# Optimization experiments

Measured on AMD Instinct MI355X. Metric: run time of the kernel, lower is better.

The kernel has to match this reference:

```python
import jax, jax.numpy as jnp
import numpy as np

IN_DIM = 1024
HEAD_DIM = 64
NUM_HEADS = 16
SEQ = 4096


def setup_inputs() -> dict:
    key = jax.random.key(0)
    ks = jax.random.split(key, 7)
    s = 1.0 / np.sqrt(IN_DIM)
    return {
        "h": jax.random.normal(ks[0], (SEQ, IN_DIM), dtype=jnp.float32),
        "Wq": jax.random.uniform(ks[1], (IN_DIM, NUM_HEADS * HEAD_DIM), jnp.float32, -s, s),
        "Wk": jax.random.uniform(ks[2], (IN_DIM, NUM_HEADS * HEAD_DIM), jnp.float32, -s, s),
        "Wv": jax.random.uniform(ks[3], (IN_DIM, NUM_HEADS * HEAD_DIM), jnp.float32, -s, s),
        "bq": jax.random.uniform(ks[4], (NUM_HEADS * HEAD_DIM,), jnp.float32, -s, s),
        "bk": jax.random.uniform(ks[5], (NUM_HEADS * HEAD_DIM,), jnp.float32, -s, s),
        "bv": jax.random.uniform(ks[6], (NUM_HEADS * HEAD_DIM,), jnp.float32, -s, s),
    }


def reference(h, Wq, Wk, Wv, bq, bk, bv):
    n = h.shape[0]
    # QKV projections -> [H, S, D]
    q = (h @ Wq + bq).reshape(n, NUM_HEADS, HEAD_DIM).transpose(1, 0, 2)
    k = (h @ Wk + bk).reshape(n, NUM_HEADS, HEAD_DIM).transpose(1, 0, 2)
    v = (h @ Wv + bv).reshape(n, NUM_HEADS, HEAD_DIM).transpose(1, 0, 2)
    scale = 1.0 / np.sqrt(HEAD_DIM).astype(np.float32)
    scores = jnp.einsum('hsd,htd->hst', q, k) * scale  # [H, S, S]
    probs = jax.nn.softmax(scores, axis=-1)
    out = jnp.einsum('hst,htd->hsd', probs, v)  # [H, S, D]
    return out.transpose(1, 0, 2).reshape(n, NUM_HEADS * HEAD_DIM)
```

## Files before the change

### kernel.cpp

```cpp
#include <hip/hip_runtime.h>
#include <hip/hip_bf16.h>

#define IN_DIM    1024
#define HEAD_DIM  64
#define NUM_HEADS 16
#define SEQ       4096

#define QSCALE 0.18033688011112042f

typedef __bf16 bf16;
typedef __attribute__((ext_vector_type(4))) __bf16 bf16x4;
typedef __attribute__((ext_vector_type(8))) __bf16 bf16x8;
typedef __attribute__((ext_vector_type(4))) float floatx4;

__device__ __forceinline__ void async16(bf16* lds, const bf16* g) {
    __builtin_amdgcn_global_load_lds(
        (const __attribute__((address_space(1))) unsigned int*)g,
        (__attribute__((address_space(3))) unsigned int*)lds, 16, 0, 0);
}


__global__ void mha_conv_h(const float* __restrict__ h, bf16* __restrict__ hb) {
    int i = blockIdx.x * blockDim.x + threadIdx.x;
    float4 v = ((const float4*)h)[i];
    bf16x4 r;
    r[0] = (bf16)v.x; r[1] = (bf16)v.y; r[2] = (bf16)v.z; r[3] = (bf16)v.w;
    ((bf16x4*)hb)[i] = r;
}

__global__ void mha_conv_wt(const float* __restrict__ Wq, const float* __restrict__ Wk,
                            const float* __restrict__ Wv, bf16* __restrict__ Wt) {
    __shared__ bf16 tile[64][65];
    const int mat = blockIdx.z;
    const float* W = (mat == 0) ? Wq : (mat == 1) ? Wk : Wv;
    const int k0 = blockIdx.y * 64, n0 = blockIdx.x * 64;
    const int tn = threadIdx.x & 63, tq = threadIdx.x >> 6;
#pragma unroll
    for (int i = 0; i < 16; ++i) {
        int kk = tq + i * 4;
        tile[kk][tn] = (bf16)W[(size_t)(k0 + kk) * 1024 + n0 + tn];
    }
    __syncthreads();
#pragma unroll
    for (int i = 0; i < 16; ++i) {
        int nn = tq + i * 4;
        Wt[((size_t)mat << 20) + (size_t)(n0 + nn) * 1024 + k0 + tn] = tile[tn][nn];
    }
}

__launch_bounds__(256)
__global__ void mha_qkv_gemm(const bf16* __restrict__ hb, const bf16* __restrict__ Wt,
                             const float* __restrict__ bq, const float* __restrict__ bk,
                             const float* __restrict__ bv,
                             bf16* __restrict__ Qb, bf16* __restrict__ Kb,
                             bf16* __restrict__ Vt) {
    __shared__ __align__(16) bf16 As[128 * 32];
    __shared__ __align__(16) bf16 Bs[128 * 32];

    const int lane = threadIdx.x & 63;
    const int wave = threadIdx.x >> 6;
    const int l16  = lane & 15;
    const int quad = lane >> 4;
    const int wm   = wave & 1;
    const int wn   = wave >> 1;

    const int m0  = blockIdx.x * 128;
    const int n0  = blockIdx.y * 128;
    const int mat = n0 >> 10;
    const int nc0 = n0 & 1023;

    const bf16* Wp = Wt + ((size_t)mat << 20);

    floatx4 acc[4][4] = {};
    const int swz = (l16 >> 1) & 3;

    for (int k0 = 0; k0 < IN_DIM; k0 += 32) {
#pragma unroll
        for (int r = 0; r < 2; ++r) {
            int g = wave * 128 + r * 64 + lane;
            int row = g >> 2, c = g & 3;
            int gc = c ^ ((row >> 1) & 3);
            bf16* ldsbase_a = As + (size_t)(wave * 128 + r * 64) * 8;
            bf16* ldsbase_b = Bs + (size_t)(wave * 128 + r * 64) * 8;
            async16(ldsbase_a, hb + (size_t)(m0 + row) * IN_DIM + k0 + gc * 8);
            async16(ldsbase_b, Wp + (size_t)(nc0 + row) * IN_DIM + k0 + gc * 8);
        }
        __syncthreads();

        bf16x8 af[4], bf[4];
#pragma unroll
        for (int mt = 0; mt < 4; ++mt)
            af[mt] = *(const bf16x8*)(As + (size_t)(wm * 64 + mt * 16 + l16) * 32
                                      + ((quad ^ swz) * 8));
#pragma unroll
        for (int nt = 0; nt < 4; ++nt)
            bf[nt] = *(const bf16x8*)(Bs + (size_t)(wn * 64 + nt * 16 + l16) * 32
                                      + ((quad ^ swz) * 8));
#pragma unroll
        for (int mt = 0; mt < 4; ++mt)
#pragma unroll
            for (int nt = 0; nt < 4; ++nt)
                acc[mt][nt] = __builtin_amdgcn_mfma_f32_16x16x32_bf16(af[mt], bf[nt],
                                                                      acc[mt][nt], 0, 0, 0);
        __syncthreads();
    }

    const float* bias = (mat == 0) ? bq : (mat == 1) ? bk : bv;
#pragma unroll
    for (int nt = 0; nt < 4; ++nt) {
        int nc = nc0 + wn * 64 + nt * 16 + l16;
        float bb = bias[nc];
        int head = nc >> 6, d = nc & 63;
#pragma unroll
        for (int mt = 0; mt < 4; ++mt)
#pragma unroll
            for (int r = 0; r < 4; ++r) {
                int srow = m0 + wm * 64 + mt * 16 + quad * 4 + r;
                float v = acc[mt][nt][r] + bb;
                if (mat == 0)
                    Qb[((size_t)head * SEQ + srow) * HEAD_DIM + d] = (bf16)(v * QSCALE);
                else if (mat == 1)
                    Kb[((size_t)head * SEQ + srow) * HEAD_DIM + d] = (bf16)v;
                else
                    Vt[((size_t)head * HEAD_DIM + d) * SEQ + srow] = (bf16)v;
            }
    }
}

__launch_bounds__(512)
__global__ void mha_attn(const bf16* __restrict__ Qb, const bf16* __restrict__ Kb,
                         const bf16* __restrict__ Vt, float* __restrict__ out) {
    __shared__ __align__(16) bf16 Ks[2][64 * 64];
    __shared__ __align__(16) bf16 Vs[2][64 * 64];
    __shared__ __align__(16) bf16 Ps[8][16 * 72];

    const int lane = threadIdx.x & 63;
    const int wave = threadIdx.x >> 6;
    const int l16  = lane & 15;
    const int quad = lane >> 4;

    const int hh    = blockIdx.y;
    const int qbase = blockIdx.x * 128 + wave * 16;

    const bf16* Qh = Qb + (size_t)hh * SEQ * HEAD_DIM;
    const bf16* Kh = Kb + (size_t)hh * SEQ * HEAD_DIM;
    const bf16* Vh = Vt + (size_t)hh * HEAD_DIM * SEQ;

    const int sg   = wave * 64 + lane;
    const int srow = sg >> 3;
    const int sgc  = (sg & 7) ^ (srow & 7);

    bf16x8 qf[2];
#pragma unroll
    for (int ks = 0; ks < 2; ++ks)
        qf[ks] = *(const bf16x8*)(Qh + (size_t)(qbase + l16) * HEAD_DIM + ks * 32 + quad * 8);

    bf16x8 vone;
#pragma unroll
    for (int i = 0; i < 8; ++i) vone[i] = (bf16)1.0f;

    floatx4 o[4] = {};
    floatx4 ol   = {};

    bf16* lp = &Ps[wave][0];
    const int swk = l16 & 7;

    async16(&Ks[0][wave * 512], Kh + (size_t)srow * HEAD_DIM + sgc * 8);
    async16(&Vs[0][wave * 512], Vh + (size_t)srow * SEQ + sgc * 8);
    __syncthreads();

    for (int t0 = 0; t0 < SEQ; t0 += 64) {
        const int cur = (t0 >> 6) & 1, nxt = cur ^ 1;
        if (t0 + 64 < SEQ) {
            async16(&Ks[nxt][wave * 512], Kh + (size_t)(t0 + 64 + srow) * HEAD_DIM + sgc * 8);
            async16(&Vs[nxt][wave * 512], Vh + (size_t)srow * SEQ + t0 + 64 + sgc * 8);
        }

        bf16x8 kf[4][2], vf[4][2];
#pragma unroll
        for (int tt = 0; tt < 4; ++tt)
#pragma unroll
            for (int ks = 0; ks < 2; ++ks)
                kf[tt][ks] = *(const bf16x8*)(&Ks[cur][(size_t)(tt * 16 + l16) * 64
                                              + (((ks * 4 + quad) ^ swk) * 8)]);
#pragma unroll
        for (int dt = 0; dt < 4; ++dt)
#pragma unroll
            for (int ks = 0; ks < 2; ++ks)
                vf[dt][ks] = *(const bf16x8*)(&Vs[cur][(size_t)(dt * 16 + l16) * 64
                                              + (((ks * 4 + quad) ^ swk) * 8)]);

#pragma unroll
        for (int tt = 0; tt < 4; ++tt) {
            floatx4 s = {};
            s = __builtin_amdgcn_mfma_f32_16x16x32_bf16(kf[tt][0], qf[0], s, 0, 0, 0);
            s = __builtin_amdgcn_mfma_f32_16x16x32_bf16(kf[tt][1], qf[1], s, 0, 0, 0);
            bf16x4 pk;
#pragma unroll
            for (int r = 0; r < 4; ++r) pk[r] = (bf16)__builtin_amdgcn_exp2f(s[r]);
            *(bf16x4*)(lp + l16 * 72 + tt * 16 + quad * 4) = pk;
        }

#pragma unroll
        for (int ks = 0; ks < 2; ++ks) {
            bf16x8 pf = *(const bf16x8*)(lp + l16 * 72 + ks * 32 + quad * 8);
#pragma unroll
            for (int dt = 0; dt < 4; ++dt)
                o[dt] = __builtin_amdgcn_mfma_f32_16x16x32_bf16(pf, vf[dt][ks], o[dt], 0, 0, 0);
            ol = __builtin_amdgcn_mfma_f32_16x16x32_bf16(pf, vone, ol, 0, 0, 0);
        }
        __syncthreads();
    }

#pragma unroll
    for (int r = 0; r < 4; ++r) {
        float inv = 1.0f / ol[r];
        int srow_o = qbase + quad * 4 + r;
#pragma unroll
        for (int dt = 0; dt < 4; ++dt)
            out[(size_t)srow_o * (NUM_HEADS * HEAD_DIM) + hh * 64 + dt * 16 + l16]
                = o[dt][r] * inv;
    }
}

extern "C" void kernel_launch(void* const* d_in, const int* in_sizes, int n_in,
                              void* d_out, int out_size, void* d_ws, size_t ws_size,
                              hipStream_t stream) {
    const float* h  = (const float*)d_in[0];
    const float* Wq = (const float*)d_in[1];
    const float* Wk = (const float*)d_in[2];
    const float* Wv = (const float*)d_in[3];
    const float* bq = (const float*)d_in[4];
    const float* bk = (const float*)d_in[5];
    const float* bv = (const float*)d_in[6];
    float* out = (float*)d_out;

    char* ws = (char*)d_ws;
    const size_t MB = 1024 * 1024;
    bf16* hb = (bf16*)(ws);
    bf16* Wt = (bf16*)(ws + 8 * MB);
    bf16* Qb = (bf16*)(ws + 14 * MB);
    bf16* Kb = (bf16*)(ws + 22 * MB);
    bf16* Vt = (bf16*)(ws + 30 * MB);

    mha_conv_h<<<(SEQ * IN_DIM / 4) / 256, 256, 0, stream>>>(h, hb);
    mha_conv_wt<<<dim3(16, 16, 3), 256, 0, stream>>>(Wq, Wk, Wv, Wt);
    mha_qkv_gemm<<<dim3(SEQ / 128, (3 * IN_DIM) / 128), 256, 0, stream>>>(
        hb, Wt, bq, bk, bv, Qb, Kb, Vt);
    mha_attn<<<dim3(SEQ / 128, NUM_HEADS), 512, 0, stream>>>(Qb, Kb, Vt, out);
}
```

Before: 204.2 us.

## Software-pipeline attention S and PV stages, transpose V projection stores

The attention loop is restructured so the QK^T/exp stage for tile t runs alongside the PV stage for tile t-1. P uses double-buffered LDS and V uses a triple buffer, and K/V fragments are loaded from LDS just before use rather than up front, which lowers register pressure. Launch bounds now request 4 blocks per SM. Separately, the V projection swaps the MFMA operands so that Vt stores are contiguous along the sequence dimension instead of strided. The cost is more LDS use and more complex buffer indexing.

```diff
diff --git a/kernel.cpp b/kernel.cpp
--- a/kernel.cpp
+++ b/kernel.cpp
@@ -73,6 +73,7 @@
 
     floatx4 acc[4][4] = {};
     const int swz = (l16 >> 1) & 3;
+    const bool swap = (mat == 2);
 
     for (int k0 = 0; k0 < IN_DIM; k0 += 32) {
 #pragma unroll
@@ -96,43 +97,66 @@
         for (int nt = 0; nt < 4; ++nt)
             bf[nt] = *(const bf16x8*)(Bs + (size_t)(wn * 64 + nt * 16 + l16) * 32
                                       + ((quad ^ swz) * 8));
-#pragma unroll
-        for (int mt = 0; mt < 4; ++mt)
-#pragma unroll
-            for (int nt = 0; nt < 4; ++nt)
-                acc[mt][nt] = __builtin_amdgcn_mfma_f32_16x16x32_bf16(af[mt], bf[nt],
-                                                                      acc[mt][nt], 0, 0, 0);
+        if (!swap) {
+#pragma unroll
+            for (int mt = 0; mt < 4; ++mt)
+#pragma unroll
+                for (int nt = 0; nt < 4; ++nt)
+                    acc[mt][nt] = __builtin_amdgcn_mfma_f32_16x16x32_bf16(af[mt], bf[nt],
+                                                                          acc[mt][nt], 0, 0, 0);
+        } else {
+#pragma unroll
+            for (int mt = 0; mt < 4; ++mt)
+#pragma unroll
+                for (int nt = 0; nt < 4; ++nt)
+                    acc[mt][nt] = __builtin_amdgcn_mfma_f32_16x16x32_bf16(bf[nt], af[mt],
+                                                                          acc[mt][nt], 0, 0, 0);
+        }
         __syncthreads();
     }
 
-    const float* bias = (mat == 0) ? bq : (mat == 1) ? bk : bv;
-#pragma unroll
-    for (int nt = 0; nt < 4; ++nt) {
-        int nc = nc0 + wn * 64 + nt * 16 + l16;
-        float bb = bias[nc];
-        int head = nc >> 6, d = nc & 63;
-#pragma unroll
-        for (int mt = 0; mt < 4; ++mt)
+    if (!swap) {
+        const float* bias = (mat == 0) ? bq : bk;
+#pragma unroll
+        for (int nt = 0; nt < 4; ++nt) {
+            int nc = nc0 + wn * 64 + nt * 16 + l16;
+            float bb = bias[nc];
+            int head = nc >> 6, d = nc & 63;
+#pragma unroll
+            for (int mt = 0; mt < 4; ++mt)
+#pragma unroll
+                for (int r = 0; r < 4; ++r) {
+                    int srow = m0 + wm * 64 + mt * 16 + quad * 4 + r;
+                    float v = acc[mt][nt][r] + bb;
+                    if (mat == 0)
+                        Qb[((size_t)head * SEQ + srow) * HEAD_DIM + d] = (bf16)(v * QSCALE);
+                    else
+                        Kb[((size_t)head * SEQ + srow) * HEAD_DIM + d] = (bf16)v;
+                }
+        }
+    } else {
+#pragma unroll
+        for (int nt = 0; nt < 4; ++nt)
 #pragma unroll
             for (int r = 0; r < 4; ++r) {
-                int srow = m0 + wm * 64 + mt * 16 + quad * 4 + r;
-                float v = acc[mt][nt][r] + bb;
-                if (mat == 0)
-                    Qb[((size_t)head * SEQ + srow) * HEAD_DIM + d] = (bf16)(v * QSCALE);
-                else if (mat == 1)
-                    Kb[((size_t)head * SEQ + srow) * HEAD_DIM + d] = (bf16)v;
-                else
-                    Vt[((size_t)head * HEAD_DIM + d) * SEQ + srow] = (bf16)v;
+                int n = nc0 + wn * 64 + nt * 16 + quad * 4 + r;
+                float bb = bv[n];
+                int head = n >> 6, d = n & 63;
+#pragma unroll
+                for (int mt = 0; mt < 4; ++mt) {
+                    int s = m0 + wm * 64 + mt * 16 + l16;
+                    Vt[((size_t)head * 64 + d) * SEQ + s] = (bf16)(acc[mt][nt][r] + bb);
+                }
             }
     }
 }
 
-__launch_bounds__(512)
+__launch_bounds__(512, 4)
 __global__ void mha_attn(const bf16* __restrict__ Qb, const bf16* __restrict__ Kb,
                          const bf16* __restrict__ Vt, float* __restrict__ out) {
     __shared__ __align__(16) bf16 Ks[2][64 * 64];
-    __shared__ __align__(16) bf16 Vs[2][64 * 64];
-    __shared__ __align__(16) bf16 Ps[8][16 * 72];
+    __shared__ __align__(16) bf16 Vs[3][64 * 64];
+    __shared__ __align__(16) bf16 Ps[2][8][16 * 72];
 
     const int lane = threadIdx.x & 63;
     const int wave = threadIdx.x >> 6;
@@ -162,55 +186,65 @@
     floatx4 o[4] = {};
     floatx4 ol   = {};
 
-    bf16* lp = &Ps[wave][0];
     const int swk = l16 & 7;
 
-    async16(&Ks[0][wave * 512], Kh + (size_t)srow * HEAD_DIM + sgc * 8);
-    async16(&Vs[0][wave * 512], Vh + (size_t)srow * SEQ + sgc * 8);
-    __syncthreads();
-
-    for (int t0 = 0; t0 < SEQ; t0 += 64) {
-        const int cur = (t0 >> 6) & 1, nxt = cur ^ 1;
-        if (t0 + 64 < SEQ) {
-            async16(&Ks[nxt][wave * 512], Kh + (size_t)(t0 + 64 + srow) * HEAD_DIM + sgc * 8);
-            async16(&Vs[nxt][wave * 512], Vh + (size_t)srow * SEQ + t0 + 64 + sgc * 8);
-        }
-
-        bf16x8 kf[4][2], vf[4][2];
-#pragma unroll
-        for (int tt = 0; tt < 4; ++tt)
-#pragma unroll
-            for (int ks = 0; ks < 2; ++ks)
-                kf[tt][ks] = *(const bf16x8*)(&Ks[cur][(size_t)(tt * 16 + l16) * 64
-                                              + (((ks * 4 + quad) ^ swk) * 8)]);
-#pragma unroll
-        for (int dt = 0; dt < 4; ++dt)
-#pragma unroll
-            for (int ks = 0; ks < 2; ++ks)
-                vf[dt][ks] = *(const bf16x8*)(&Vs[cur][(size_t)(dt * 16 + l16) * 64
-                                              + (((ks * 4 + quad) ^ swk) * 8)]);
-
+    auto stageK = [&](int slot, int t) {
+        async16(&Ks[slot][wave * 512], Kh + (size_t)(t * 64 + srow) * HEAD_DIM + sgc * 8);
+    };
+    auto stageV = [&](int slot, int t) {
+        async16(&Vs[slot][wave * 512], Vh + (size_t)srow * SEQ + t * 64 + sgc * 8);
+    };
+    auto doS = [&](int kslot, int pslot) {
+        bf16* lp = &Ps[pslot][wave][0];
 #pragma unroll
         for (int tt = 0; tt < 4; ++tt) {
+            bf16x8 k0 = *(const bf16x8*)(&Ks[kslot][(size_t)(tt * 16 + l16) * 64
+                                         + ((quad ^ swk) * 8)]);
+            bf16x8 k1 = *(const bf16x8*)(&Ks[kslot][(size_t)(tt * 16 + l16) * 64
+                                         + (((4 + quad) ^ swk) * 8)]);
             floatx4 s = {};
-            s = __builtin_amdgcn_mfma_f32_16x16x32_bf16(kf[tt][0], qf[0], s, 0, 0, 0);
-            s = __builtin_amdgcn_mfma_f32_16x16x32_bf16(kf[tt][1], qf[1], s, 0, 0, 0);
+            s = __builtin_amdgcn_mfma_f32_16x16x32_bf16(k0, qf[0], s, 0, 0, 0);
+            s = __builtin_amdgcn_mfma_f32_16x16x32_bf16(k1, qf[1], s, 0, 0, 0);
             bf16x4 pk;
 #pragma unroll
             for (int r = 0; r < 4; ++r) pk[r] = (bf16)__builtin_amdgcn_exp2f(s[r]);
             *(bf16x4*)(lp + l16 * 72 + tt * 16 + quad * 4) = pk;
         }
-
+    };
+    auto doPV = [&](int vslot, int pslot) {
+        bf16* lp = &Ps[pslot][wave][0];
 #pragma unroll
         for (int ks = 0; ks < 2; ++ks) {
             bf16x8 pf = *(const bf16x8*)(lp + l16 * 72 + ks * 32 + quad * 8);
 #pragma unroll
-            for (int dt = 0; dt < 4; ++dt)
-                o[dt] = __builtin_amdgcn_mfma_f32_16x16x32_bf16(pf, vf[dt][ks], o[dt], 0, 0, 0);
+            for (int dt = 0; dt < 4; ++dt) {
+                bf16x8 vf = *(const bf16x8*)(&Vs[vslot][(size_t)(dt * 16 + l16) * 64
+                                             + (((ks * 4 + quad) ^ swk) * 8)]);
+                o[dt] = __builtin_amdgcn_mfma_f32_16x16x32_bf16(pf, vf, o[dt], 0, 0, 0);
+            }
             ol = __builtin_amdgcn_mfma_f32_16x16x32_bf16(pf, vone, ol, 0, 0, 0);
         }
+    };
+
+    stageK(0, 0); stageV(0, 0);
+    __syncthreads();
+
+    stageK(1, 1); stageV(1, 1);
+    doS(0, 0);
+    __syncthreads();
+
+    int ivw = 2;
+    int ivr = 0;
+    for (int t = 1; t < 64; ++t) {
+        const int par = t & 1;
+        if (t < 63) { stageK(par ^ 1, t + 1); stageV(ivw, t + 1); }
+        doS(par, par);
+        doPV(ivr, par ^ 1);
         __syncthreads();
-    }
+        ivw = (ivw == 2) ? 0 : ivw + 1;
+        ivr = (ivr == 2) ? 0 : ivr + 1;
+    }
+    doPV(0, 1);
 
 #pragma unroll
     for (int r = 0; r < 4; ++r) {
```

After: 220.1 us. 1.08x slower.

## Give each attention wave four query tiles and coalesce the V-transpose store

Applied to the files above, without the earlier changes.

The attention kernel now runs 256-thread blocks that each cover 256 queries, so every wave owns 64 query rows (four 16-row tiles). Each K/V fragment read from LDS is then reused across four tiles, which cuts LDS traffic and K/V staging per query. In the QKV GEMM, the V path swaps the MFMA operands so the accumulator comes out transposed, turning the strided Vt stores into contiguous writes along the sequence. The trade-off is more accumulator registers per wave and fewer blocks in the grid (256 instead of 512), which can reduce occupancy.

```diff
diff --git a/kernel.cpp b/kernel.cpp
--- a/kernel.cpp
+++ b/kernel.cpp
@@ -74,65 +74,102 @@
     floatx4 acc[4][4] = {};
     const int swz = (l16 >> 1) & 3;
 
-    for (int k0 = 0; k0 < IN_DIM; k0 += 32) {
-#pragma unroll
-        for (int r = 0; r < 2; ++r) {
-            int g = wave * 128 + r * 64 + lane;
-            int row = g >> 2, c = g & 3;
-            int gc = c ^ ((row >> 1) & 3);
-            bf16* ldsbase_a = As + (size_t)(wave * 128 + r * 64) * 8;
-            bf16* ldsbase_b = Bs + (size_t)(wave * 128 + r * 64) * 8;
-            async16(ldsbase_a, hb + (size_t)(m0 + row) * IN_DIM + k0 + gc * 8);
-            async16(ldsbase_b, Wp + (size_t)(nc0 + row) * IN_DIM + k0 + gc * 8);
-        }
-        __syncthreads();
-
-        bf16x8 af[4], bf[4];
-#pragma unroll
-        for (int mt = 0; mt < 4; ++mt)
-            af[mt] = *(const bf16x8*)(As + (size_t)(wm * 64 + mt * 16 + l16) * 32
-                                      + ((quad ^ swz) * 8));
+    int g0 = wave * 128 + lane, g1 = g0 + 64;
+    int row0 = g0 >> 2, gc0 = (g0 & 3) ^ ((row0 >> 1) & 3);
+    int row1 = g1 >> 2, gc1 = (g1 & 3) ^ ((row1 >> 1) & 3);
+    bf16* la0 = As + (size_t)(wave * 128) * 8;
+    bf16* la1 = As + (size_t)(wave * 128 + 64) * 8;
+    bf16* lb0 = Bs + (size_t)(wave * 128) * 8;
+    bf16* lb1 = Bs + (size_t)(wave * 128 + 64) * 8;
+
+    if (mat != 2) {
+        for (int k0 = 0; k0 < IN_DIM; k0 += 32) {
+            async16(la0, hb + (size_t)(m0 + row0) * IN_DIM + k0 + gc0 * 8);
+            async16(la1, hb + (size_t)(m0 + row1) * IN_DIM + k0 + gc1 * 8);
+            async16(lb0, Wp + (size_t)(nc0 + row0) * IN_DIM + k0 + gc0 * 8);
+            async16(lb1, Wp + (size_t)(nc0 + row1) * IN_DIM + k0 + gc1 * 8);
+            __syncthreads();
+            bf16x8 af[4], bf[4];
+#pragma unroll
+            for (int mt = 0; mt < 4; ++mt)
+                af[mt] = *(const bf16x8*)(As + (size_t)(wm * 64 + mt * 16 + l16) * 32
+                                          + ((quad ^ swz) * 8));
+#pragma unroll
+            for (int nt = 0; nt < 4; ++nt)
+                bf[nt] = *(const bf16x8*)(Bs + (size_t)(wn * 64 + nt * 16 + l16) * 32
+                                          + ((quad ^ swz) * 8));
+#pragma unroll
+            for (int mt = 0; mt < 4; ++mt)
+#pragma unroll
+                for (int nt = 0; nt < 4; ++nt)
+                    acc[mt][nt] = __builtin_amdgcn_mfma_f32_16x16x32_bf16(af[mt], bf[nt],
+                                                                          acc[mt][nt], 0, 0, 0);
+            __syncthreads();
+        }
+        const float* bias = (mat == 0) ? bq : bk;
+#pragma unroll
+        for (int nt = 0; nt < 4; ++nt) {
+            int nc = nc0 + wn * 64 + nt * 16 + l16;
+            float bb = bias[nc];
+            int head = nc >> 6, d = nc & 63;
+#pragma unroll
+            for (int mt = 0; mt < 4; ++mt)
+#pragma unroll
+                for (int r = 0; r < 4; ++r) {
+                    int srow = m0 + wm * 64 + mt * 16 + quad * 4 + r;
+                    float v = acc[mt][nt][r] + bb;
+                    if (mat == 0)
+                        Qb[((size_t)head * SEQ + srow) * HEAD_DIM + d] = (bf16)(v * QSCALE);
+                    else
+                        Kb[((size_t)head * SEQ + srow) * HEAD_DIM + d] = (bf16)v;
+                }
+        }
+    } else {
+        for (int k0 = 0; k0 < IN_DIM; k0 += 32) {
+            async16(la0, hb + (size_t)(m0 + row0) * IN_DIM + k0 + gc0 * 8);
+            async16(la1, hb + (size_t)(m0 + row1) * IN_DIM + k0 + gc1 * 8);
+            async16(lb0, Wp + (size_t)(nc0 + row0) * IN_DIM + k0 + gc0 * 8);
+            async16(lb1, Wp + (size_t)(nc0 + row1) * IN_DIM + k0 + gc1 * 8);
+            __syncthreads();
+            bf16x8 af[4], bf[4];
+#pragma unroll
+            for (int mt = 0; mt < 4; ++mt)
+                af[mt] = *(const bf16x8*)(As + (size_t)(wm * 64 + mt * 16 + l16) * 32
+                                          + ((quad ^ swz) * 8));
+#pragma unroll
+            for (int nt = 0; nt < 4; ++nt)
+                bf[nt] = *(const bf16x8*)(Bs + (size_t)(wn * 64 + nt * 16 + l16) * 32
+                                          + ((quad ^ swz) * 8));
+#pragma unroll
+            for (int mt = 0; mt < 4; ++mt)
+#pragma unroll
+                for (int nt = 0; nt < 4; ++nt)
+                    acc[mt][nt] = __builtin_amdgcn_mfma_f32_16x16x32_bf16(bf[nt], af[mt],
+                                                                          acc[mt][nt], 0, 0, 0);
+            __syncthreads();
+        }
 #pragma unroll
         for (int nt = 0; nt < 4; ++nt)
-            bf[nt] = *(const bf16x8*)(Bs + (size_t)(wn * 64 + nt * 16 + l16) * 32
-                                      + ((quad ^ swz) * 8));
-#pragma unroll
-        for (int mt = 0; mt < 4; ++mt)
-#pragma unroll
-            for (int nt = 0; nt < 4; ++nt)
-                acc[mt][nt] = __builtin_amdgcn_mfma_f32_16x16x32_bf16(af[mt], bf[nt],
-                                                                      acc[mt][nt], 0, 0, 0);
-        __syncthreads();
-    }
-
-    const float* bias = (mat == 0) ? bq : (mat == 1) ? bk : bv;
-#pragma unroll
-    for (int nt = 0; nt < 4; ++nt) {
-        int nc = nc0 + wn * 64 + nt * 16 + l16;
-        float bb = bias[nc];
-        int head = nc >> 6, d = nc & 63;
-#pragma unroll
-        for (int mt = 0; mt < 4; ++mt)
 #pragma unroll
             for (int r = 0; r < 4; ++r) {
-                int srow = m0 + wm * 64 + mt * 16 + quad * 4 + r;
-                float v = acc[mt][nt][r] + bb;
-                if (mat == 0)
-                    Qb[((size_t)head * SEQ + srow) * HEAD_DIM + d] = (bf16)(v * QSCALE);
-                else if (mat == 1)
-                    Kb[((size_t)head * SEQ + srow) * HEAD_DIM + d] = (bf16)v;
-                else
-                    Vt[((size_t)head * HEAD_DIM + d) * SEQ + srow] = (bf16)v;
+                int n = nc0 + wn * 64 + nt * 16 + quad * 4 + r;
+                float bb = bv[n];
+                int head = n >> 6, d = n & 63;
+#pragma unroll
+                for (int mt = 0; mt < 4; ++mt) {
+                    int s = m0 + wm * 64 + mt * 16 + l16;
+                    Vt[((size_t)head * 64 + d) * SEQ + s] = (bf16)(acc[mt][nt][r] + bb);
+                }
             }
     }
 }
 
-__launch_bounds__(512)
+__launch_bounds__(256, 2)
 __global__ void mha_attn(const bf16* __restrict__ Qb, const bf16* __restrict__ Kb,
                          const bf16* __restrict__ Vt, float* __restrict__ out) {
     __shared__ __align__(16) bf16 Ks[2][64 * 64];
     __shared__ __align__(16) bf16 Vs[2][64 * 64];
-    __shared__ __align__(16) bf16 Ps[8][16 * 72];
+    __shared__ __align__(16) bf16 Ps[16][16 * 72];
 
     const int lane = threadIdx.x & 63;
     const int wave = threadIdx.x >> 6;
@@ -140,43 +177,48 @@
     const int quad = lane >> 4;
 
     const int hh    = blockIdx.y;
-    const int qbase = blockIdx.x * 128 + wave * 16;
+    const int qbase = blockIdx.x * 256 + wave * 64;
 
     const bf16* Qh = Qb + (size_t)hh * SEQ * HEAD_DIM;
     const bf16* Kh = Kb + (size_t)hh * SEQ * HEAD_DIM;
     const bf16* Vh = Vt + (size_t)hh * HEAD_DIM * SEQ;
 
-    const int sg   = wave * 64 + lane;
-    const int srow = sg >> 3;
-    const int sgc  = (sg & 7) ^ (srow & 7);
-
-    bf16x8 qf[2];
-#pragma unroll
-    for (int ks = 0; ks < 2; ++ks)
-        qf[ks] = *(const bf16x8*)(Qh + (size_t)(qbase + l16) * HEAD_DIM + ks * 32 + quad * 8);
+    const int g0 = wave * 128 + lane, g1 = g0 + 64;
+    const int sr0 = g0 >> 3, sc0 = (g0 & 7) ^ (sr0 & 7);
+    const int sr1 = g1 >> 3, sc1 = (g1 & 7) ^ (sr1 & 7);
+
+    bf16x8 qf[4][2];
+#pragma unroll
+    for (int m = 0; m < 4; ++m)
+#pragma unroll
+        for (int ks = 0; ks < 2; ++ks)
+            qf[m][ks] = *(const bf16x8*)(Qh + (size_t)(qbase + m * 16 + l16) * HEAD_DIM
+                                         + ks * 32 + quad * 8);
 
     bf16x8 vone;
 #pragma unroll
     for (int i = 0; i < 8; ++i) vone[i] = (bf16)1.0f;
 
-    floatx4 o[4] = {};
-    floatx4 ol   = {};
-
-    bf16* lp = &Ps[wave][0];
+    floatx4 o[4][4] = {};
+    floatx4 ol[4]   = {};
+
     const int swk = l16 & 7;
 
-    async16(&Ks[0][wave * 512], Kh + (size_t)srow * HEAD_DIM + sgc * 8);
-    async16(&Vs[0][wave * 512], Vh + (size_t)srow * SEQ + sgc * 8);
+    auto stage = [&](int slot, int t) {
+        async16(&Ks[slot][(wave * 128) * 8],      Kh + (size_t)(t * 64 + sr0) * HEAD_DIM + sc0 * 8);
+        async16(&Ks[slot][(wave * 128 + 64) * 8], Kh + (size_t)(t * 64 + sr1) * HEAD_DIM + sc1 * 8);
+        async16(&Vs[slot][(wave * 128) * 8],      Vh + (size_t)sr0 * SEQ + t * 64 + sc0 * 8);
+        async16(&Vs[slot][(wave * 128 + 64) * 8], Vh + (size_t)sr1 * SEQ + t * 64 + sc1 * 8);
+    };
+
+    stage(0, 0);
     __syncthreads();
 
-    for (int t0 = 0; t0 < SEQ; t0 += 64) {
-        const int cur = (t0 >> 6) & 1, nxt = cur ^ 1;
-        if (t0 + 64 < SEQ) {
-            async16(&Ks[nxt][wave * 512], Kh + (size_t)(t0 + 64 + srow) * HEAD_DIM + sgc * 8);
-            async16(&Vs[nxt][wave * 512], Vh + (size_t)srow * SEQ + t0 + 64 + sgc * 8);
-        }
-
-        bf16x8 kf[4][2], vf[4][2];
+    for (int t = 0; t < 64; ++t) {
+        const int cur = t & 1;
+        if (t < 63) stage(cur ^ 1, t + 1);
+
+        bf16x8 kf[4][2];
 #pragma unroll
         for (int tt = 0; tt < 4; ++tt)
 #pragma unroll
@@ -184,43 +226,54 @@
                 kf[tt][ks] = *(const bf16x8*)(&Ks[cur][(size_t)(tt * 16 + l16) * 64
                                               + (((ks * 4 + quad) ^ swk) * 8)]);
 #pragma unroll
+        for (int m = 0; m < 4; ++m) {
+            bf16* lp = &Ps[wave * 4 + m][0];
+#pragma unroll
+            for (int tt = 0; tt < 4; ++tt) {
+                floatx4 s = {};
+                s = __builtin_amdgcn_mfma_f32_16x16x32_bf16(kf[tt][0], qf[m][0], s, 0, 0, 0);
+                s = __builtin_amdgcn_mfma_f32_16x16x32_bf16(kf[tt][1], qf[m][1], s, 0, 0, 0);
+                bf16x4 pk;
+#pragma unroll
+                for (int r = 0; r < 4; ++r) pk[r] = (bf16)__builtin_amdgcn_exp2f(s[r]);
+                *(bf16x4*)(lp + l16 * 72 + tt * 16 + quad * 4) = pk;
+            }
+        }
+
+        bf16x8 vf[4][2];
+#pragma unroll
         for (int dt = 0; dt < 4; ++dt)
 #pragma unroll
             for (int ks = 0; ks < 2; ++ks)
                 vf[dt][ks] = *(const bf16x8*)(&Vs[cur][(size_t)(dt * 16 + l16) * 64
                                               + (((ks * 4 + quad) ^ swk) * 8)]);
-
-#pragma unroll
-        for (int tt = 0; tt < 4; ++tt) {
-            floatx4 s = {};
-            s = __builtin_amdgcn_mfma_f32_16x16x32_bf16(kf[tt][0], qf[0], s, 0, 0, 0);
-            s = __builtin_amdgcn_mfma_f32_16x16x32_bf16(kf[tt][1], qf[1], s, 0, 0, 0);
-            bf16x4 pk;
-#pragma unroll
-            for (int r = 0; r < 4; ++r) pk[r] = (bf16)__builtin_amdgcn_exp2f(s[r]);
-            *(bf16x4*)(lp + l16 * 72 + tt * 16 + quad * 4) = pk;
-        }
-
-#pragma unroll
-        for (int ks = 0; ks < 2; ++ks) {
-            bf16x8 pf = *(const bf16x8*)(lp + l16 * 72 + ks * 32 + quad * 8);
-#pragma unroll
-            for (int dt = 0; dt < 4; ++dt)
-                o[dt] = __builtin_amdgcn_mfma_f32_16x16x32_bf16(pf, vf[dt][ks], o[dt], 0, 0, 0);
-            ol = __builtin_amdgcn_mfma_f32_16x16x32_bf16(pf, vone, ol, 0, 0, 0);
+#pragma unroll
+        for (int m = 0; m < 4; ++m) {
+            bf16* lp = &Ps[wave * 4 + m][0];
+#pragma unroll
+            for (int ks = 0; ks < 2; ++ks) {
+                bf16x8 pf = *(const bf16x8*)(lp + l16 * 72 + ks * 32 + quad * 8);
+#pragma unroll
+                for (int dt = 0; dt < 4; ++dt)
+                    o[m][dt] = __builtin_amdgcn_mfma_f32_16x16x32_bf16(pf, vf[dt][ks],
+                                                                       o[m][dt], 0, 0, 0);
+                ol[m] = __builtin_amdgcn_mfma_f32_16x16x32_bf16(pf, vone, ol[m], 0, 0, 0);
+            }
         }
         __syncthreads();
     }
 
 #pragma unroll
-    for (int r = 0; r < 4; ++r) {
-        float inv = 1.0f / ol[r];
-        int srow_o = qbase + quad * 4 + r;
-#pragma unroll
-        for (int dt = 0; dt < 4; ++dt)
-            out[(size_t)srow_o * (NUM_HEADS * HEAD_DIM) + hh * 64 + dt * 16 + l16]
-                = o[dt][r] * inv;
-    }
+    for (int m = 0; m < 4; ++m)
+#pragma unroll
+        for (int r = 0; r < 4; ++r) {
+            float inv = 1.0f / ol[m][r];
+            int srow_o = qbase + m * 16 + quad * 4 + r;
+#pragma unroll
+            for (int dt = 0; dt < 4; ++dt)
+                out[(size_t)srow_o * (NUM_HEADS * HEAD_DIM) + hh * 64 + dt * 16 + l16]
+                    = o[m][dt][r] * inv;
+        }
 }
 
 extern "C" void kernel_launch(void* const* d_in, const int* in_sizes, int n_in,
@@ -247,5 +300,5 @@
     mha_conv_wt<<<dim3(16, 16, 3), 256, 0, stream>>>(Wq, Wk, Wv, Wt);
     mha_qkv_gemm<<<dim3(SEQ / 128, (3 * IN_DIM) / 128), 256, 0, stream>>>(
         hb, Wt, bq, bk, bv, Qb, Kb, Vt);
-    mha_attn<<<dim3(SEQ / 128, NUM_HEADS), 512, 0, stream>>>(Qb, Kb, Vt, out);
-}
+    mha_attn<<<dim3(SEQ / 256, NUM_HEADS), 256, 0, stream>>>(Qb, Kb, Vt, out);
+}
```

New measurement: 233.1 us. +14.1%, slower.
